# Performance work log

Measured on AMD Instinct MI355X. Metric: run time of the kernel, lower is better.

## Reference

```python
import jax, jax.numpy as jnp
import numpy as np

IN_F = 4096
OUT_F = 4096
GS = 128  # group size for int4 scales


def setup_inputs() -> dict:
    key = jax.random.key(0)
    ks = jax.random.split(key, 5)
    x = jax.random.normal(ks[0], (4, 2048, IN_F), dtype=jnp.float32)
    # each byte packs two unsigned int4 values (low nibble = even col, high nibble = odd col)
    w_packed = jax.random.randint(ks[1], (OUT_F, IN_F // 2), 0, 256, dtype=jnp.int32)
    w_scales = jax.random.uniform(ks[2], (OUT_F, IN_F // GS), dtype=jnp.float32,
                                  minval=0.005, maxval=0.02)
    perm = jax.random.permutation(ks[3], IN_F).astype(jnp.int32)
    bias = jax.random.normal(ks[4], (OUT_F,), dtype=jnp.float32) * 0.01
    return {"x": x, "w_packed": w_packed, "w_scales": w_scales, "perm": perm, "bias": bias}


def _dequantize_groupwise_int4(w_packed, w_scales):
    # unpack two int4 values per byte, zero-point 8 -> symmetric range [-8, 7]
    low = (w_packed & 0xF) - 8
    high = ((w_packed >> 4) & 0xF) - 8
    q = jnp.stack([low, high], axis=-1).reshape(OUT_F, IN_F).astype(jnp.float32)
    # apply one scale per group of GS input features
    w = q.reshape(OUT_F, IN_F // GS, GS) * w_scales[:, :, None]
    return w.reshape(OUT_F, IN_F)  # [out_features, in_features]


def reference(x, w_packed, w_scales, perm, bias):
    shape = x.shape
    xf = x.reshape(-1, IN_F)[:, perm]          # activation permutation (GPTQ act-order)
    w = _dequantize_groupwise_int4(w_packed, w_scales)
    y = xf @ w.T                               # [tokens, out_features]
    return y.reshape(*shape[:-1], OUT_F) + bias
```

## Files before the change

kernel.cpp:

```cpp
#include <hip/hip_runtime.h>

#define IN_F 4096
#define OUT_F 4096
#define GS 128

#define BM 256
#define BN 256
#define BKB 128
#define NT (IN_F / BKB)
#define BUFB (BM * BKB)

typedef int i32x4 __attribute__((ext_vector_type(4)));

typedef __attribute__((address_space(1))) void void_g;
typedef __attribute__((address_space(3))) void void_l;

__device__ __forceinline__ void async_copy16(void* lds, const void* g) {
  __builtin_amdgcn_global_load_lds((const void_g*)g, (void_l*)lds, 16, 0, 0);
}

__device__ __forceinline__ void stage_g(signed char* region, int rowbase,
                                        const signed char* mat, int k0,
                                        int wave, int growl, int gcolb) {
  async_copy16(region + rowbase * BKB + wave * 1024,
               mat + (size_t)(rowbase + growl) * IN_F + k0 + gcolb);
}

__global__ void invperm_kernel(const int* __restrict__ perm, int* __restrict__ inv) {
  int i = blockIdx.x * blockDim.x + threadIdx.x;
  inv[perm[i]] = i;
}

__global__ __launch_bounds__(256) void prep_kernel(
    const float* __restrict__ x,
    unsigned int* __restrict__ xq4,
    float* __restrict__ sx,
    const int* __restrict__ wp,
    const float* __restrict__ wsc,
    const int* __restrict__ inv,
    unsigned int* __restrict__ wq4,
    float* __restrict__ sw,
    int M)
{
  __shared__ unsigned int prow[IN_F / 2];
  __shared__ float srow[IN_F / GS];
  __shared__ float red[256];
  const int tid = threadIdx.x;
  const int b = blockIdx.x;

  if (b < M) {
    const float4* x4 = (const float4*)(x + (size_t)b * IN_F);
    float4 v[4];
    float m = 0.f;
#pragma unroll
    for (int i = 0; i < 4; ++i) {
      v[i] = x4[tid + i * 256];
      m = fmaxf(m, fmaxf(fmaxf(fabsf(v[i].x), fabsf(v[i].y)),
                         fmaxf(fabsf(v[i].z), fabsf(v[i].w))));
    }
    red[tid] = m;
    __syncthreads();
#pragma unroll
    for (int s = 128; s > 0; s >>= 1) {
      if (tid < s) red[tid] = fmaxf(red[tid], red[tid + s]);
      __syncthreads();
    }
    const float mx = red[0];
    const float r = 127.0f / mx;
    if (tid == 0) sx[b] = mx * (1.0f / 127.0f);

    unsigned int* orow = xq4 + (size_t)b * (IN_F / 4);
#pragma unroll
    for (int i = 0; i < 4; ++i) {
      int q0 = (int)rintf(v[i].x * r);
      int q1 = (int)rintf(v[i].y * r);
      int q2 = (int)rintf(v[i].z * r);
      int q3 = (int)rintf(v[i].w * r);
      orow[tid + i * 256] = (unsigned)(q0 & 0xFF) | ((unsigned)(q1 & 0xFF) << 8) |
                            ((unsigned)(q2 & 0xFF) << 16) | ((unsigned)(q3 & 0xFF) << 24);
    }
  } else {
    const int o = b - M;
    const int4* wp4 = (const int4*)(wp + (size_t)o * (IN_F / 2));
    int4* p4 = (int4*)prow;
#pragma unroll
    for (int i = 0; i < 2; ++i)
      p4[tid + i * 256] = wp4[tid + i * 256];
    if (tid < IN_F / GS) srow[tid] = wsc[o * (IN_F / GS) + tid];
    __syncthreads();

    float m = 0.f;
#pragma unroll
    for (int c = 0; c < 8; ++c) {
      const int p = tid + c * 256;
      const unsigned bb = prow[p];
      const float s = srow[p >> 6];
      const float lo = (float)((int)(bb & 0xFu) - 8);
      const float hi = (float)((int)((bb >> 4) & 0xFu) - 8);
      m = fmaxf(m, fmaxf(fabsf(lo), fabsf(hi)) * s);
    }
    red[tid] = m;
    __syncthreads();
#pragma unroll
    for (int s = 128; s > 0; s >>= 1) {
      if (tid < s) red[tid] = fmaxf(red[tid], red[tid + s]);
      __syncthreads();
    }
    const float wmax = red[0];
    const float r = (wmax > 0.f) ? 127.0f / wmax : 0.f;
    if (tid == 0) sw[o] = wmax * (1.0f / 127.0f);

    unsigned int* orow = wq4 + (size_t)o * (IN_F / 4);
    const int4* inv4 = (const int4*)inv;
#pragma unroll
    for (int c = 0; c < 4; ++c) {
      const int p = tid + c * 256;
      const int4 iv = inv4[p];
      unsigned out = 0;
      const int idx[4] = {iv.x, iv.y, iv.z, iv.w};
#pragma unroll
      for (int e = 0; e < 4; ++e) {
        const int ii = idx[e];
        const unsigned wbits = prow[ii >> 1];
        const int n = (int)((wbits >> ((ii & 1) * 4)) & 0xFu) - 8;
        const float v = (float)n * srow[ii >> 7] * r;
        const int q = (int)rintf(v);
        out |= (unsigned)(q & 0xFF) << (e * 8);
      }
      orow[p] = out;
    }
  }
}

template <bool LAST>
__device__ __forceinline__ void gemm_tile(
    const signed char* Ac, const signed char* Bc,
    signed char* An, signed char* Bn,
    const signed char* a_base, const signed char* b_base, int k0n,
    int wave, int wm, int wn, int l16, int quad, int sxz,
    int growl, int gcolb, i32x4 (&aq)[2][2][2], i32x4 (&bq)[4][2],
    i32x4 (&acc)[8][4])
{
#pragma unroll
  for (int p = 0; p < 4; ++p) {
    const int cb = p & 1;
    const int nb = cb ^ 1;
    if (p == 0) {
#pragma unroll
      for (int j = 0; j < 4; ++j)
#pragma unroll
        for (int ks = 0; ks < 2; ++ks)
          bq[j][ks] = *(const i32x4*)(Bc + (wn + j * 16 + l16) * BKB +
                                      ((ks * 64 + quad * 16) ^ sxz));
      __builtin_amdgcn_sched_barrier(0);
    }
    if (p < 3) {
#pragma unroll
      for (int i = 0; i < 2; ++i)
#pragma unroll
        for (int ks = 0; ks < 2; ++ks)
          aq[nb][i][ks] = *(const i32x4*)(Ac + (wm + (p + 1) * 32 + i * 16 + l16) * BKB +
                                          ((ks * 64 + quad * 16) ^ sxz));
    } else if (!LAST) {
#pragma unroll
      for (int i = 0; i < 2; ++i)
#pragma unroll
        for (int ks = 0; ks < 2; ++ks)
          aq[nb][i][ks] = *(const i32x4*)(An + (wm + i * 16 + l16) * BKB +
                                          ((ks * 64 + quad * 16) ^ sxz));
    }
    __builtin_amdgcn_sched_barrier(0);
    if (!LAST) {
      if (p == 0) {
        stage_g(Bn, 0, b_base, k0n, wave, growl, gcolb);
        stage_g(Bn, 64, b_base, k0n, wave, growl, gcolb);
      } else if (p == 1) {
        stage_g(An, 0, a_base, k0n, wave, growl, gcolb);
        stage_g(An, 128, a_base, k0n, wave, growl, gcolb);
      } else if (p == 2) {
        stage_g(Bn, 128, b_base, k0n, wave, growl, gcolb);
        stage_g(Bn, 192, b_base, k0n, wave, growl, gcolb);
      } else {
        stage_g(An, 64, a_base, k0n, wave, growl, gcolb);
        stage_g(An, 192, a_base, k0n, wave, growl, gcolb);
      }
    }
    if (p == 3 && LAST) { asm volatile("s_waitcnt lgkmcnt(0)" ::: "memory"); }
    else                { asm volatile("s_waitcnt lgkmcnt(4)" ::: "memory"); }
    __builtin_amdgcn_sched_barrier(0);
    __builtin_amdgcn_s_setprio(1);
#pragma unroll
    for (int i = 0; i < 2; ++i)
#pragma unroll
      for (int j = 0; j < 4; ++j)
#pragma unroll
        for (int ks = 0; ks < 2; ++ks)
          acc[2 * p + i][j] = __builtin_amdgcn_mfma_i32_16x16x64_i8(
              aq[cb][i][ks], bq[j][ks], acc[2 * p + i][j], 0, 0, 0);
    __builtin_amdgcn_s_setprio(0);
    if (p == 0) {
      if (LAST) { asm volatile("s_waitcnt vmcnt(0)" ::: "memory"); }
      else      { asm volatile("s_waitcnt vmcnt(2)" ::: "memory"); }
      __builtin_amdgcn_sched_barrier(0);
      __builtin_amdgcn_s_barrier();
    } else if (p == 2 && !LAST) {
      asm volatile("s_waitcnt vmcnt(2)" ::: "memory");
      __builtin_amdgcn_sched_barrier(0);
      __builtin_amdgcn_s_barrier();
    } else if (p == 3) {
      if (!LAST) { asm volatile("s_waitcnt vmcnt(2)" ::: "memory"); }
      __builtin_amdgcn_sched_barrier(0);
      __builtin_amdgcn_s_barrier();
    }
  }
}

__global__ __launch_bounds__(512, 2) void gemm_kernel(
    const signed char* __restrict__ A,
    const signed char* __restrict__ B,
    const float* __restrict__ sx,
    const float* __restrict__ sw,
    const float* __restrict__ bias,
    float* __restrict__ C) {
  __shared__ __align__(16) signed char As[2 * BUFB];
  __shared__ __align__(16) signed char Bs[2 * BUFB];

  const int tid  = threadIdx.x;
  const int wave = tid >> 6;
  const int lane = tid & 63;
  const int quad = lane >> 4;
  const int l16  = lane & 15;

  const int bm = blockIdx.y;
  const int bn = blockIdx.x;
  const signed char* a_base = A + (size_t)bm * BM * IN_F;
  const signed char* b_base = B + (size_t)bn * BN * IN_F;

  const int wm = (wave >> 2) * 128;
  const int wn = (wave & 3) * 64;
  const int sxz = (l16 & 7) << 4;

  const int growl = tid >> 3;
  const int gcolb = ((tid & 7) ^ ((tid >> 3) & 7)) << 4;

  i32x4 acc[8][4] = {};
  i32x4 aq[2][2][2];
  i32x4 bq[4][2];

  stage_g(Bs, 0, b_base, 0, wave, growl, gcolb);
  stage_g(Bs, 64, b_base, 0, wave, growl, gcolb);
  stage_g(Bs, 128, b_base, 0, wave, growl, gcolb);
  stage_g(Bs, 192, b_base, 0, wave, growl, gcolb);
  stage_g(As, 0, a_base, 0, wave, growl, gcolb);
  stage_g(As, 128, a_base, 0, wave, growl, gcolb);
  stage_g(As, 64, a_base, 0, wave, growl, gcolb);
  stage_g(As, 192, a_base, 0, wave, growl, gcolb);
  asm volatile("s_waitcnt vmcnt(2)" ::: "memory");
  __builtin_amdgcn_sched_barrier(0);
  __builtin_amdgcn_s_barrier();

#pragma unroll
  for (int i = 0; i < 2; ++i)
#pragma unroll
    for (int ks = 0; ks < 2; ++ks)
      aq[0][i][ks] = *(const i32x4*)(As + (wm + i * 16 + l16) * BKB +
                                     ((ks * 64 + quad * 16) ^ sxz));

#pragma unroll 1
  for (int t = 0; t < NT - 1; ++t) {
    const int cur = t & 1;
    const int nxt = cur ^ 1;
    gemm_tile<false>(As + cur * BUFB, Bs + cur * BUFB,
                     As + nxt * BUFB, Bs + nxt * BUFB,
                     a_base, b_base, (t + 1) * BKB,
                     wave, wm, wn, l16, quad, sxz, growl, gcolb, aq, bq, acc);
  }
  gemm_tile<true>(As + ((NT - 1) & 1) * BUFB, Bs + ((NT - 1) & 1) * BUFB,
                  nullptr, nullptr, a_base, b_base, 0,
                  wave, wm, wn, l16, quad, sxz, growl, gcolb, aq, bq, acc);

  float* sxs = (float*)As;
  float* sws = sxs + BM;
  float* bsh = sws + BN;
  if (tid < BM) {
    sxs[tid] = sx[bm * BM + tid];
  } else {
    const int c = tid - BM;
    sws[c] = sw[bn * BN + c];
    bsh[c] = bias[bn * BN + c];
  }
  __syncthreads();

  const int wm_g = bm * BM + wm;
  const int wn_g = bn * BN + wn;
#pragma unroll
  for (int j = 0; j < 4; ++j) {
    const int col_l = wn + j * 16 + l16;
    const float swv = sws[col_l];
    const float bv  = bsh[col_l];
    const int col = wn_g + j * 16 + l16;
#pragma unroll
    for (int i = 0; i < 8; ++i) {
      const int row_l0 = wm + i * 16 + quad * 4;
      const int row0 = wm_g + i * 16 + quad * 4;
#pragma unroll
      for (int r = 0; r < 4; ++r)
        C[(size_t)(row0 + r) * OUT_F + col] =
            (float)acc[i][j][r] * (sxs[row_l0 + r] * swv) + bv;
    }
  }
}

extern "C" void kernel_launch(void* const* d_in, const int* in_sizes, int n_in,
                              void* d_out, int out_size, void* d_ws, size_t ws_size,
                              hipStream_t stream) {
  const float* x    = (const float*)d_in[0];
  const int*   wp   = (const int*)d_in[1];
  const float* wsc  = (const float*)d_in[2];
  const int*   perm = (const int*)d_in[3];
  const float* bias = (const float*)d_in[4];
  float* out = (float*)d_out;

  const int M = in_sizes[0] / IN_F;

  signed char* xq = (signed char*)d_ws;
  signed char* wq = xq + (size_t)M * IN_F;
  float* sx = (float*)(wq + (size_t)OUT_F * IN_F);
  float* sw = sx + M;
  int* inv = (int*)(sw + OUT_F);

  invperm_kernel<<<IN_F / 256, 256, 0, stream>>>(perm, inv);

  prep_kernel<<<M + OUT_F, 256, 0, stream>>>(
      x, (unsigned int*)xq, sx, wp, wsc, inv, (unsigned int*)wq, sw, M);

  dim3 grid(OUT_F / BN, M / BM);
  gemm_kernel<<<grid, 512, 0, stream>>>(xq, wq, sx, sw, bias, out);
}
```

Measured before the change: 377.4 us.

## Permute activations instead of weights, drop inverse-perm kernel, unroll GEMM ping-pong

The activation permutation now happens during x quantization: each row is staged in shared memory and gathered through perm. Weights are quantized in natural order with contiguous nibble unpacking, so the per-element random gather in the weight path goes away. The inverse-permutation kernel and its launch are removed. The GEMM main loop is unrolled by two with compile-time buffer indices and precomputed LDS offsets to cut address arithmetic. The cost is 16KB of extra shared memory in the prep kernel, which may lower its occupancy.

```diff
diff --git a/kernel.cpp b/kernel.cpp
--- a/kernel.cpp
+++ b/kernel.cpp
@@ -24,11 +24,6 @@
                                         int wave, int growl, int gcolb) {
   async_copy16(region + rowbase * BKB + wave * 1024,
                mat + (size_t)(rowbase + growl) * IN_F + k0 + gcolb);
-}
-
-__global__ void invperm_kernel(const int* __restrict__ perm, int* __restrict__ inv) {
-  int i = blockIdx.x * blockDim.x + threadIdx.x;
-  inv[perm[i]] = i;
 }
 
 __global__ __launch_bounds__(256) void prep_kernel(
@@ -37,11 +32,12 @@
     float* __restrict__ sx,
     const int* __restrict__ wp,
     const float* __restrict__ wsc,
-    const int* __restrict__ inv,
+    const int* __restrict__ perm,
     unsigned int* __restrict__ wq4,
     float* __restrict__ sw,
     int M)
 {
+  __shared__ float xrow[IN_F];
   __shared__ unsigned int prow[IN_F / 2];
   __shared__ float srow[IN_F / GS];
   __shared__ float red[256];
@@ -50,13 +46,14 @@
 
   if (b < M) {
     const float4* x4 = (const float4*)(x + (size_t)b * IN_F);
-    float4 v[4];
+    float4* xr4 = (float4*)xrow;
     float m = 0.f;
 #pragma unroll
     for (int i = 0; i < 4; ++i) {
-      v[i] = x4[tid + i * 256];
-      m = fmaxf(m, fmaxf(fmaxf(fabsf(v[i].x), fabsf(v[i].y)),
-                         fmaxf(fabsf(v[i].z), fabsf(v[i].w))));
+      float4 v = x4[tid + i * 256];
+      xr4[tid + i * 256] = v;
+      m = fmaxf(m, fmaxf(fmaxf(fabsf(v.x), fabsf(v.y)),
+                         fmaxf(fabsf(v.z), fabsf(v.w))));
     }
     red[tid] = m;
     __syncthreads();
@@ -70,14 +67,17 @@
     if (tid == 0) sx[b] = mx * (1.0f / 127.0f);
 
     unsigned int* orow = xq4 + (size_t)b * (IN_F / 4);
-#pragma unroll
-    for (int i = 0; i < 4; ++i) {
-      int q0 = (int)rintf(v[i].x * r);
-      int q1 = (int)rintf(v[i].y * r);
-      int q2 = (int)rintf(v[i].z * r);
-      int q3 = (int)rintf(v[i].w * r);
-      orow[tid + i * 256] = (unsigned)(q0 & 0xFF) | ((unsigned)(q1 & 0xFF) << 8) |
-                            ((unsigned)(q2 & 0xFF) << 16) | ((unsigned)(q3 & 0xFF) << 24);
+    const int4* perm4 = (const int4*)perm;
+#pragma unroll
+    for (int c = 0; c < 4; ++c) {
+      const int p = tid + c * 256;
+      const int4 pv = perm4[p];
+      int q0 = (int)rintf(xrow[pv.x] * r);
+      int q1 = (int)rintf(xrow[pv.y] * r);
+      int q2 = (int)rintf(xrow[pv.z] * r);
+      int q3 = (int)rintf(xrow[pv.w] * r);
+      orow[p] = (unsigned)(q0 & 0xFF) | ((unsigned)(q1 & 0xFF) << 8) |
+                ((unsigned)(q2 & 0xFF) << 16) | ((unsigned)(q3 & 0xFF) << 24);
     }
   } else {
     const int o = b - M;
@@ -111,36 +111,35 @@
     if (tid == 0) sw[o] = wmax * (1.0f / 127.0f);
 
     unsigned int* orow = wq4 + (size_t)o * (IN_F / 4);
-    const int4* inv4 = (const int4*)inv;
 #pragma unroll
     for (int c = 0; c < 4; ++c) {
       const int p = tid + c * 256;
-      const int4 iv = inv4[p];
-      unsigned out = 0;
-      const int idx[4] = {iv.x, iv.y, iv.z, iv.w};
-#pragma unroll
-      for (int e = 0; e < 4; ++e) {
-        const int ii = idx[e];
-        const unsigned wbits = prow[ii >> 1];
-        const int n = (int)((wbits >> ((ii & 1) * 4)) & 0xFu) - 8;
-        const float v = (float)n * srow[ii >> 7] * r;
-        const int q = (int)rintf(v);
-        out |= (unsigned)(q & 0xFF) << (e * 8);
-      }
-      orow[p] = out;
-    }
-  }
-}
-
-template <bool LAST>
+      const unsigned b0 = prow[2 * p];
+      const unsigned b1 = prow[2 * p + 1];
+      const float s = srow[p >> 5] * r;
+      int q0 = (int)rintf((float)((int)(b0 & 0xFu) - 8) * s);
+      int q1 = (int)rintf((float)((int)((b0 >> 4) & 0xFu) - 8) * s);
+      int q2 = (int)rintf((float)((int)(b1 & 0xFu) - 8) * s);
+      int q3 = (int)rintf((float)((int)((b1 >> 4) & 0xFu) - 8) * s);
+      orow[p] = (unsigned)(q0 & 0xFF) | ((unsigned)(q1 & 0xFF) << 8) |
+                ((unsigned)(q2 & 0xFF) << 16) | ((unsigned)(q3 & 0xFF) << 24);
+    }
+  }
+}
+
+template <int CUR, bool LAST>
 __device__ __forceinline__ void gemm_tile(
-    const signed char* Ac, const signed char* Bc,
-    signed char* An, signed char* Bn,
+    signed char* As, signed char* Bs,
     const signed char* a_base, const signed char* b_base, int k0n,
-    int wave, int wm, int wn, int l16, int quad, int sxz,
+    int wave, int a_row, int b_row, const int (&lp)[2],
     int growl, int gcolb, i32x4 (&aq)[2][2][2], i32x4 (&bq)[4][2],
     i32x4 (&acc)[8][4])
 {
+  const signed char* a_l  = As + CUR * BUFB + a_row;
+  const signed char* b_l  = Bs + CUR * BUFB + b_row;
+  const signed char* an_l = As + (CUR ^ 1) * BUFB + a_row;
+  signed char* Anw = As + (CUR ^ 1) * BUFB;
+  signed char* Bnw = Bs + (CUR ^ 1) * BUFB;
 #pragma unroll
   for (int p = 0; p < 4; ++p) {
     const int cb = p & 1;
@@ -150,8 +149,7 @@
       for (int j = 0; j < 4; ++j)
 #pragma unroll
         for (int ks = 0; ks < 2; ++ks)
-          bq[j][ks] = *(const i32x4*)(Bc + (wn + j * 16 + l16) * BKB +
-                                      ((ks * 64 + quad * 16) ^ sxz));
+          bq[j][ks] = *(const i32x4*)(b_l + j * 16 * BKB + lp[ks]);
       __builtin_amdgcn_sched_barrier(0);
     }
     if (p < 3) {
@@ -159,30 +157,28 @@
       for (int i = 0; i < 2; ++i)
 #pragma unroll
         for (int ks = 0; ks < 2; ++ks)
-          aq[nb][i][ks] = *(const i32x4*)(Ac + (wm + (p + 1) * 32 + i * 16 + l16) * BKB +
-                                          ((ks * 64 + quad * 16) ^ sxz));
+          aq[nb][i][ks] = *(const i32x4*)(a_l + ((p + 1) * 32 + i * 16) * BKB + lp[ks]);
     } else if (!LAST) {
 #pragma unroll
       for (int i = 0; i < 2; ++i)
 #pragma unroll
         for (int ks = 0; ks < 2; ++ks)
-          aq[nb][i][ks] = *(const i32x4*)(An + (wm + i * 16 + l16) * BKB +
-                                          ((ks * 64 + quad * 16) ^ sxz));
+          aq[nb][i][ks] = *(const i32x4*)(an_l + i * 16 * BKB + lp[ks]);
     }
     __builtin_amdgcn_sched_barrier(0);
     if (!LAST) {
       if (p == 0) {
-        stage_g(Bn, 0, b_base, k0n, wave, growl, gcolb);
-        stage_g(Bn, 64, b_base, k0n, wave, growl, gcolb);
+        stage_g(Bnw, 0, b_base, k0n, wave, growl, gcolb);
+        stage_g(Bnw, 64, b_base, k0n, wave, growl, gcolb);
       } else if (p == 1) {
-        stage_g(An, 0, a_base, k0n, wave, growl, gcolb);
-        stage_g(An, 128, a_base, k0n, wave, growl, gcolb);
+        stage_g(Anw, 0, a_base, k0n, wave, growl, gcolb);
+        stage_g(Anw, 128, a_base, k0n, wave, growl, gcolb);
       } else if (p == 2) {
-        stage_g(Bn, 128, b_base, k0n, wave, growl, gcolb);
-        stage_g(Bn, 192, b_base, k0n, wave, growl, gcolb);
+        stage_g(Bnw, 128, b_base, k0n, wave, growl, gcolb);
+        stage_g(Bnw, 192, b_base, k0n, wave, growl, gcolb);
       } else {
-        stage_g(An, 64, a_base, k0n, wave, growl, gcolb);
-        stage_g(An, 192, a_base, k0n, wave, growl, gcolb);
+        stage_g(Anw, 64, a_base, k0n, wave, growl, gcolb);
+        stage_g(Anw, 192, a_base, k0n, wave, growl, gcolb);
       }
     }
     if (p == 3 && LAST) { asm volatile("s_waitcnt lgkmcnt(0)" ::: "memory"); }
@@ -239,6 +235,11 @@
   const int wm = (wave >> 2) * 128;
   const int wn = (wave & 3) * 64;
   const int sxz = (l16 & 7) << 4;
+  int lp[2];
+#pragma unroll
+  for (int ks = 0; ks < 2; ++ks) lp[ks] = (ks * 64 + quad * 16) ^ sxz;
+  const int a_row = (wm + l16) * BKB;
+  const int b_row = (wn + l16) * BKB;
 
   const int growl = tid >> 3;
   const int gcolb = ((tid & 7) ^ ((tid >> 3) & 7)) << 4;
@@ -263,21 +264,19 @@
   for (int i = 0; i < 2; ++i)
 #pragma unroll
     for (int ks = 0; ks < 2; ++ks)
-      aq[0][i][ks] = *(const i32x4*)(As + (wm + i * 16 + l16) * BKB +
-                                     ((ks * 64 + quad * 16) ^ sxz));
+      aq[0][i][ks] = *(const i32x4*)(As + a_row + i * 16 * BKB + lp[ks]);
 
 #pragma unroll 1
-  for (int t = 0; t < NT - 1; ++t) {
-    const int cur = t & 1;
-    const int nxt = cur ^ 1;
-    gemm_tile<false>(As + cur * BUFB, Bs + cur * BUFB,
-                     As + nxt * BUFB, Bs + nxt * BUFB,
-                     a_base, b_base, (t + 1) * BKB,
-                     wave, wm, wn, l16, quad, sxz, growl, gcolb, aq, bq, acc);
-  }
-  gemm_tile<true>(As + ((NT - 1) & 1) * BUFB, Bs + ((NT - 1) & 1) * BUFB,
-                  nullptr, nullptr, a_base, b_base, 0,
-                  wave, wm, wn, l16, quad, sxz, growl, gcolb, aq, bq, acc);
+  for (int t = 0; t + 2 <= NT - 1; t += 2) {
+    gemm_tile<0, false>(As, Bs, a_base, b_base, (t + 1) * BKB,
+                        wave, a_row, b_row, lp, growl, gcolb, aq, bq, acc);
+    gemm_tile<1, false>(As, Bs, a_base, b_base, (t + 2) * BKB,
+                        wave, a_row, b_row, lp, growl, gcolb, aq, bq, acc);
+  }
+  gemm_tile<0, false>(As, Bs, a_base, b_base, (NT - 1) * BKB,
+                      wave, a_row, b_row, lp, growl, gcolb, aq, bq, acc);
+  gemm_tile<1, true>(As, Bs, a_base, b_base, 0,
+                     wave, a_row, b_row, lp, growl, gcolb, aq, bq, acc);
 
   float* sxs = (float*)As;
   float* sws = sxs + BM;
@@ -327,12 +326,9 @@
   signed char* wq = xq + (size_t)M * IN_F;
   float* sx = (float*)(wq + (size_t)OUT_F * IN_F);
   float* sw = sx + M;
-  int* inv = (int*)(sw + OUT_F);
-
-  invperm_kernel<<<IN_F / 256, 256, 0, stream>>>(perm, inv);
 
   prep_kernel<<<M + OUT_F, 256, 0, stream>>>(
-      x, (unsigned int*)xq, sx, wp, wsc, inv, (unsigned int*)wq, sw, M);
+      x, (unsigned int*)xq, sx, wp, wsc, perm, (unsigned int*)wq, sw, M);
 
   dim3 grid(OUT_F / BN, M / BM);
   gemm_kernel<<<grid, 512, 0, stream>>>(xq, wq, sx, sw, bias, out);
```

Result: faster. 368.2 us (-2.4%).
